# Kernel optimization log

Measured on AMD Instinct MI355X. Metric: run time of the kernel, lower is better.

The kernel has to match this reference:

```python
import jax, jax.numpy as jnp
import numpy as np

M = 8        # number of input features
NMF = 4      # membership functions per feature
R = NMF ** M # 65536 rules
N = 1024     # batch size


def setup_inputs() -> dict:
    key = jax.random.key(0)
    k1, k2, k3, k4, k5 = jax.random.split(key, 5)
    x = jax.random.normal(k1, (N, M), dtype=jnp.float32)
    # Antecedent parameters: torch.rand -> uniform [0,1)
    center = jax.random.uniform(k2, (M, NMF), dtype=jnp.float32)
    sigma = jax.random.uniform(k3, (M, NMF), dtype=jnp.float32)
    # Consequent linear layer, init_Consequent uses uniform [0,1)
    W = jax.random.uniform(k4, (R, M), dtype=jnp.float32)
    b = jax.random.uniform(k5, (R,), dtype=jnp.float32)
    return {"x": x, "center": center, "sigma": sigma, "W": W, "b": b}


def reference(x, center, sigma, W, b):
    # droprule=False (deterministic reference; the torch drop_rule is random Bernoulli masking)
    n = x.shape[0]
    # Gaussian membership, faithful to torch: exp(-(x - c)^2 / 2 * sigma^2)
    # mg: [N, M, NMF]
    mg = jnp.exp(-((x[:, :, None] - center[None, :, :]) ** 2) * 0.5 * (sigma[None, :, :] ** 2))
    # Combinatorial rule product via mixed-radix broadcasting:
    # fg[n, r] = prod_m mg[n, m, digit_m(r)], feature 0 most significant.
    fg = mg[:, 0, :]  # [N, NMF]
    for m in range(1, M):
        fg = (fg[:, :, None] * mg[:, m, None, :]).reshape(n, -1)
    # fg: [N, R]
    fg_bar = fg / jnp.sum(fg, axis=1, keepdims=True)
    rule_out = x @ W.T + b  # [N, R]
    return jnp.sum(fg_bar * rule_out, axis=1)  # [N]
```

## Files before the change

kernel.cpp:

```cpp
#include <hip/hip_runtime.h>
#include <hip/hip_bf16.h>

typedef __attribute__((ext_vector_type(8))) short short8;
typedef __attribute__((ext_vector_type(4))) float f32x4;

#define KB 32
#define HPB 8
#define ROWP 16

__device__ __forceinline__ ushort f2bf(float f) {
    __hip_bfloat16 h = __float2bfloat16(f);
    return *reinterpret_cast<ushort*>(&h);
}
__device__ __forceinline__ unsigned pk2(float a, float b) {
    return (unsigned)f2bf(a) | ((unsigned)f2bf(b) << 16);
}

__global__ __launch_bounds__(256, 8) void fz_main(
    const float* __restrict__ x, const float* __restrict__ center,
    const float* __restrict__ sigma, const float* __restrict__ W,
    const float* __restrict__ b, float* __restrict__ S , int N)
{
    __shared__ float  mgs[16][33];
    __shared__ float  pr[16][20] __attribute__((aligned(16)));
    __shared__ ushort plf[8][64][8] __attribute__((aligned(16)));
    __shared__ float  phs[16][HPB + 1];
    __shared__ float  red[4][16][9];

    const int t = threadIdx.x;
    const int tile = blockIdx.x >> 5;
    const int kb = blockIdx.x & (KB - 1);

    #pragma unroll
    for (int v = 0; v < 2; ++v) {
        int id = t + v * 256;
        int s = id >> 5, i = id & 31, m = i >> 2;
        float xv = x[(size_t)(tile * 16 + s) * 8 + m];
        float d = xv - center[i];
        float sg = sigma[i];
        mgs[s][i] = __expf(-d * d * 0.5f * sg * sg);
    }
    __syncthreads();
    {
        int s = t >> 4, a = t & 15;
        pr[s][a] = mgs[s][24 + (a >> 2)] * mgs[s][28 + (a & 3)];
        if (a < HPB) {
            int hi = kb * HPB + a;
            phs[s][a] = mgs[s][hi >> 6] * mgs[s][4 + ((hi >> 4) & 3)]
                      * mgs[s][8 + ((hi >> 2) & 3)] * mgs[s][12 + (hi & 3)];
        }
    }
    __syncthreads();
    {
        const int ls = t >> 5;
        #pragma unroll
        for (int oct = 0; oct < 2; ++oct) {
            const int lane_e = (2 * t + oct) & 63;
            const int s = lane_e & 15;
            const int hi3 = lane_e >> 4;
            const int L0 = ls * 32 + hi3 * 8;
            const float pqv = mgs[s][16 + (L0 >> 6)] * mgs[s][20 + ((L0 >> 4) & 3)];
            const int b7 = L0 & 8;
            const float4 r0 = *reinterpret_cast<const float4*>(&pr[s][b7]);
            const float4 r1 = *reinterpret_cast<const float4*>(&pr[s][b7 + 4]);
            unsigned Pk[4] = { pk2(pqv * r0.x, pqv * r0.y), pk2(pqv * r0.z, pqv * r0.w),
                               pk2(pqv * r1.x, pqv * r1.y), pk2(pqv * r1.z, pqv * r1.w) };
            *reinterpret_cast<short8*>(&plf[ls][lane_e][0]) =
                *reinterpret_cast<short8*>(&Pk[0]);
        }
    }
    __syncthreads();

    const int wv = t >> 6, lane = t & 63;
    const int c = lane & 15, kb4 = lane >> 4;

    const float* src = (c < 8) ? (W + c) : b;
    const int stride = (c < 8) ? 8 : 1;
    const unsigned lmask = (c <= 8) ? 0xFFFFFFFFu : 0u;

    const int hi_base = kb * HPB + wv * 2;
    const float* p = src + (size_t)(hi_base * 256 + kb4 * 8) * stride;
    const ptrdiff_t s32 = (ptrdiff_t)32 * stride;

    float bufA[8], bufB[8];
    #pragma unroll
    for (int j = 0; j < 8; ++j) bufA[j] = p[j * stride];

    f32x4 master = {0.f, 0.f, 0.f, 0.f};
    f32x4 d = {0.f, 0.f, 0.f, 0.f};
    #pragma unroll
    for (int step = 0; step < 16; ++step) {
        const float* pn = p + s32;
        float* nxt = (step & 1) ? bufA : bufB;
        if (step < 15) {
            #pragma unroll
            for (int j = 0; j < 8; ++j) nxt[j] = pn[j * stride];
        }
        const float* cu = (step & 1) ? bufB : bufA;
        unsigned Bp[4] = { pk2(cu[0], cu[1]) & lmask, pk2(cu[2], cu[3]) & lmask,
                           pk2(cu[4], cu[5]) & lmask, pk2(cu[6], cu[7]) & lmask };
        short8 B = *reinterpret_cast<short8*>(&Bp[0]);
        short8 A = *reinterpret_cast<const short8*>(&plf[step & 7][lane][0]);
        d = __builtin_amdgcn_mfma_f32_16x16x32_bf16(A, B, d, 0, 0, 0);
        if ((step & 7) == 7) {
            const int hil = step >> 3;
            #pragma unroll
            for (int r = 0; r < 4; ++r)
                master[r] += phs[kb4 * 4 + r][wv * 2 + hil] * d[r];
            d = (f32x4){0.f, 0.f, 0.f, 0.f};
        }
        p = pn;
    }

    if (c < 9) {
        #pragma unroll
        for (int r = 0; r < 4; ++r)
            red[wv][kb4 * 4 + r][c] = master[r];
    }
    __syncthreads();
    if (t < 144) {
        int s = t / 9, cc = t % 9;
        float v = red[0][s][cc] + red[1][s][cc] + red[2][s][cc] + red[3][s][cc];
        S[((size_t)kb * N + tile * 16 + s) * ROWP + cc] = v;
    }
}

__global__ __launch_bounds__(64) void fz_final(
    const float* __restrict__ x, const float* __restrict__ center,
    const float* __restrict__ sigma, const float* __restrict__ S,
    float* __restrict__ out, int N)
{
    int n = blockIdx.x * 64 + threadIdx.x;
    if (n >= N) return;
    float xv[8];
    #pragma unroll
    for (int m = 0; m < 8; ++m) xv[m] = x[(size_t)n * 8 + m];
    float denom = 1.f;
    #pragma unroll
    for (int m = 0; m < 8; ++m) {
        float ssum = 0.f;
        #pragma unroll
        for (int j = 0; j < 4; ++j) {
            float dd = xv[m] - center[m * 4 + j];
            float sg = sigma[m * 4 + j];
            ssum += __expf(-dd * dd * 0.5f * sg * sg);
        }
        denom *= ssum;
    }
    float sc[9];
    #pragma unroll
    for (int cc = 0; cc < 9; ++cc) sc[cc] = 0.f;
    #pragma unroll
    for (int ch = 0; ch < KB; ++ch) {
        const float* p = S + ((size_t)ch * N + n) * ROWP;
        const float4 a  = *reinterpret_cast<const float4*>(p);
        const float4 bq = *reinterpret_cast<const float4*>(p + 4);
        sc[0] += a.x;  sc[1] += a.y;  sc[2] += a.z;  sc[3] += a.w;
        sc[4] += bq.x; sc[5] += bq.y; sc[6] += bq.z; sc[7] += bq.w;
        sc[8] += p[8];
    }
    float num = sc[8];
    #pragma unroll
    for (int m = 0; m < 8; ++m) num += xv[m] * sc[m];
    out[n] = num / denom;
}

extern "C" void kernel_launch(void* const* d_in, const int* in_sizes, int n_in,
                              void* d_out, int out_size, void* d_ws, size_t ws_size,
                              hipStream_t stream)
{
    const float* x      = (const float*)d_in[0];
    const float* center = (const float*)d_in[1];
    const float* sigma  = (const float*)d_in[2];
    const float* W      = (const float*)d_in[3];
    const float* b      = (const float*)d_in[4];
    float* out = (float*)d_out;
    const int N = in_sizes[0] / 8;

    float* S = (float*)d_ws;

    fz_main<<<(N / 16) * KB, 256, 0, stream>>>(x, center, sigma, W, b, S, N);
    fz_final<<<(N + 63) / 64, 64, 0, stream>>>(x, center, sigma, S, out, N);
}
```

Measured before the change: 79.90 us.

## Fuse final reduction into main kernel via atomics and halve K-split

Drops the second finalize kernel and the workspace round-trip. Each block now computes its own normalizer and partial numerator and atomically adds into the output, which is zeroed with a memset first. The K-split goes from 32 to 16 blocks per tile, so each wave runs 32 MFMA steps instead of 16, and the A fragments are hoisted into registers. The cost is fewer blocks (less parallelism), atomics with non-deterministic summation order, an extra memset launch, and no occupancy hint in the launch bounds.

```diff
diff --git a/kernel.cpp b/kernel.cpp
--- a/kernel.cpp
+++ b/kernel.cpp
@@ -4,9 +4,7 @@
 typedef __attribute__((ext_vector_type(8))) short short8;
 typedef __attribute__((ext_vector_type(4))) float f32x4;
 
-#define KB 32
-#define HPB 8
-#define ROWP 16
+#define KB 16
 
 __device__ __forceinline__ ushort f2bf(float f) {
     __hip_bfloat16 h = __float2bfloat16(f);
@@ -16,27 +14,32 @@
     return (unsigned)f2bf(a) | ((unsigned)f2bf(b) << 16);
 }
 
-__global__ __launch_bounds__(256, 8) void fz_main(
+__global__ __launch_bounds__(256) void fz_main(
     const float* __restrict__ x, const float* __restrict__ center,
     const float* __restrict__ sigma, const float* __restrict__ W,
-    const float* __restrict__ b, float* __restrict__ S , int N)
+    const float* __restrict__ b, float* __restrict__ out, int N)
 {
+    __shared__ float  xs[16][9];
     __shared__ float  mgs[16][33];
     __shared__ float  pr[16][20] __attribute__((aligned(16)));
     __shared__ ushort plf[8][64][8] __attribute__((aligned(16)));
-    __shared__ float  phs[16][HPB + 1];
+    __shared__ float  phs[16][17];
     __shared__ float  red[4][16][9];
 
     const int t = threadIdx.x;
-    const int tile = blockIdx.x >> 5;
+    const int tile = blockIdx.x >> 4;
     const int kb = blockIdx.x & (KB - 1);
 
+    if (t < 128) {
+        int s = t >> 3, m = t & 7;
+        xs[s][m] = x[(size_t)(tile * 16 + s) * 8 + m];
+    }
+    __syncthreads();
     #pragma unroll
     for (int v = 0; v < 2; ++v) {
         int id = t + v * 256;
         int s = id >> 5, i = id & 31, m = i >> 2;
-        float xv = x[(size_t)(tile * 16 + s) * 8 + m];
-        float d = xv - center[i];
+        float d = xs[s][m] - center[i];
         float sg = sigma[i];
         mgs[s][i] = __expf(-d * d * 0.5f * sg * sg);
     }
@@ -44,11 +47,9 @@
     {
         int s = t >> 4, a = t & 15;
         pr[s][a] = mgs[s][24 + (a >> 2)] * mgs[s][28 + (a & 3)];
-        if (a < HPB) {
-            int hi = kb * HPB + a;
-            phs[s][a] = mgs[s][hi >> 6] * mgs[s][4 + ((hi >> 4) & 3)]
-                      * mgs[s][8 + ((hi >> 2) & 3)] * mgs[s][12 + (hi & 3)];
-        }
+        int hi = kb * KB + a;
+        phs[s][a] = mgs[s][hi >> 6] * mgs[s][4 + ((hi >> 4) & 3)]
+                  * mgs[s][8 + ((hi >> 2) & 3)] * mgs[s][12 + (hi & 3)];
     }
     __syncthreads();
     {
@@ -73,12 +74,16 @@
 
     const int wv = t >> 6, lane = t & 63;
     const int c = lane & 15, kb4 = lane >> 4;
+    short8 A[8];
+    #pragma unroll
+    for (int ls = 0; ls < 8; ++ls)
+        A[ls] = *reinterpret_cast<const short8*>(&plf[ls][lane][0]);
 
     const float* src = (c < 8) ? (W + c) : b;
     const int stride = (c < 8) ? 8 : 1;
     const unsigned lmask = (c <= 8) ? 0xFFFFFFFFu : 0u;
 
-    const int hi_base = kb * HPB + wv * 2;
+    const int hi_base = kb * KB + wv * 4;
     const float* p = src + (size_t)(hi_base * 256 + kb4 * 8) * stride;
     const ptrdiff_t s32 = (ptrdiff_t)32 * stride;
 
@@ -89,10 +94,10 @@
     f32x4 master = {0.f, 0.f, 0.f, 0.f};
     f32x4 d = {0.f, 0.f, 0.f, 0.f};
     #pragma unroll
-    for (int step = 0; step < 16; ++step) {
+    for (int step = 0; step < 32; ++step) {
         const float* pn = p + s32;
         float* nxt = (step & 1) ? bufA : bufB;
-        if (step < 15) {
+        if (step < 31) {
             #pragma unroll
             for (int j = 0; j < 8; ++j) nxt[j] = pn[j * stride];
         }
@@ -100,13 +105,12 @@
         unsigned Bp[4] = { pk2(cu[0], cu[1]) & lmask, pk2(cu[2], cu[3]) & lmask,
                            pk2(cu[4], cu[5]) & lmask, pk2(cu[6], cu[7]) & lmask };
         short8 B = *reinterpret_cast<short8*>(&Bp[0]);
-        short8 A = *reinterpret_cast<const short8*>(&plf[step & 7][lane][0]);
-        d = __builtin_amdgcn_mfma_f32_16x16x32_bf16(A, B, d, 0, 0, 0);
+        d = __builtin_amdgcn_mfma_f32_16x16x32_bf16(A[step & 7], B, d, 0, 0, 0);
         if ((step & 7) == 7) {
             const int hil = step >> 3;
             #pragma unroll
             for (int r = 0; r < 4; ++r)
-                master[r] += phs[kb4 * 4 + r][wv * 2 + hil] * d[r];
+                master[r] += phs[kb4 * 4 + r][wv * 4 + hil] * d[r];
             d = (f32x4){0.f, 0.f, 0.f, 0.f};
         }
         p = pn;
@@ -120,49 +124,21 @@
     __syncthreads();
     if (t < 144) {
         int s = t / 9, cc = t % 9;
-        float v = red[0][s][cc] + red[1][s][cc] + red[2][s][cc] + red[3][s][cc];
-        S[((size_t)kb * N + tile * 16 + s) * ROWP + cc] = v;
+        red[0][s][cc] += red[1][s][cc] + red[2][s][cc] + red[3][s][cc];
     }
-}
-
-__global__ __launch_bounds__(64) void fz_final(
-    const float* __restrict__ x, const float* __restrict__ center,
-    const float* __restrict__ sigma, const float* __restrict__ S,
-    float* __restrict__ out, int N)
-{
-    int n = blockIdx.x * 64 + threadIdx.x;
-    if (n >= N) return;
-    float xv[8];
-    #pragma unroll
-    for (int m = 0; m < 8; ++m) xv[m] = x[(size_t)n * 8 + m];
-    float denom = 1.f;
-    #pragma unroll
-    for (int m = 0; m < 8; ++m) {
-        float ssum = 0.f;
+    __syncthreads();
+    if (t < 16) {
+        const int s = t;
+        float denom = 1.f;
         #pragma unroll
-        for (int j = 0; j < 4; ++j) {
-            float dd = xv[m] - center[m * 4 + j];
-            float sg = sigma[m * 4 + j];
-            ssum += __expf(-dd * dd * 0.5f * sg * sg);
-        }
-        denom *= ssum;
+        for (int m = 0; m < 8; ++m)
+            denom *= (mgs[s][4 * m] + mgs[s][4 * m + 1] +
+                      mgs[s][4 * m + 2] + mgs[s][4 * m + 3]);
+        float num = red[0][s][8];
+        #pragma unroll
+        for (int m = 0; m < 8; ++m) num += xs[s][m] * red[0][s][m];
+        atomicAdd(&out[tile * 16 + s], num / denom);
     }
-    float sc[9];
-    #pragma unroll
-    for (int cc = 0; cc < 9; ++cc) sc[cc] = 0.f;
-    #pragma unroll
-    for (int ch = 0; ch < KB; ++ch) {
-        const float* p = S + ((size_t)ch * N + n) * ROWP;
-        const float4 a  = *reinterpret_cast<const float4*>(p);
-        const float4 bq = *reinterpret_cast<const float4*>(p + 4);
-        sc[0] += a.x;  sc[1] += a.y;  sc[2] += a.z;  sc[3] += a.w;
-        sc[4] += bq.x; sc[5] += bq.y; sc[6] += bq.z; sc[7] += bq.w;
-        sc[8] += p[8];
-    }
-    float num = sc[8];
-    #pragma unroll
-    for (int m = 0; m < 8; ++m) num += xv[m] * sc[m];
-    out[n] = num / denom;
 }
 
 extern "C" void kernel_launch(void* const* d_in, const int* in_sizes, int n_in,
@@ -177,8 +153,6 @@
     float* out = (float*)d_out;
     const int N = in_sizes[0] / 8;
 
-    float* S = (float*)d_ws;
-
-    fz_main<<<(N / 16) * KB, 256, 0, stream>>>(x, center, sigma, W, b, S, N);
-    fz_final<<<(N + 63) / 64, 64, 0, stream>>>(x, center, sigma, S, out, N);
+    hipMemsetAsync(out, 0, (size_t)out_size * sizeof(float), stream);
+    fz_main<<<(N / 16) * KB, 256, 0, stream>>>(x, center, sigma, W, b, out, N);
 }
```

New measurement: 77.85 us. -2.6%, faster.
